# Optimization experiments

Measured on AMD Instinct MI355X. Metric: run time of the kernel, lower is better.

The kernel has to match this reference:

```python
import jax, jax.numpy as jnp
import numpy as np

N = 50000      # nodes
E = 800000     # edges
DIN = 128      # input feature dim
H = 4          # heads
D = 16         # per-head output dim
NEG_SLOPE = 0.2


def setup_inputs() -> dict:
    key = jax.random.key(0)
    k1, k2, k3, k4, k5, k6 = jax.random.split(key, 6)
    h = jax.random.normal(k1, (N, DIN), dtype=jnp.float32)
    W = jax.random.normal(k2, (DIN, H * D), dtype=jnp.float32) * 0.05
    attn_l = jax.random.normal(k3, (H, D), dtype=jnp.float32) * 0.1
    attn_r = jax.random.normal(k4, (H, D), dtype=jnp.float32) * 0.1
    src = jax.random.randint(k5, (E,), 0, N, dtype=jnp.int32)
    dst = jax.random.randint(k6, (E,), 0, N, dtype=jnp.int32)
    return {"h": h, "W": W, "attn_l": attn_l, "attn_r": attn_r, "src": src, "dst": dst}


def reference(h, W, attn_l, attn_r, src, dst):
    n = h.shape[0]
    # linear projection: [N, H, D]
    feat = (h @ W).reshape(n, H, D)
    # per-node attention halves: [N, H]
    el = jnp.einsum('nhd,hd->nh', feat, attn_l)
    er = jnp.einsum('nhd,hd->nh', feat, attn_r)
    # per-edge logits: [E, H]
    e = jax.nn.leaky_relu(el[src] + er[dst], negative_slope=NEG_SLOPE)
    # segment softmax grouped by destination node
    m = jax.ops.segment_max(e, dst, num_segments=n)          # [N, H]
    ex = jnp.exp(e - m[dst])                                  # [E, H]
    denom = jax.ops.segment_sum(ex, dst, num_segments=n)     # [N, H]
    a = ex / denom[dst]                                       # [E, H]
    # weighted aggregation of source features: [E, H, D] -> [N, H, D]
    msg = a[:, :, None] * feat[src]
    out = jax.ops.segment_sum(msg, dst, num_segments=n)
    # mean over heads (the wrapper's .mean(1)): [N, D]
    return out.mean(axis=1)
```

## Files before the change

### kernel.cpp

```cpp
#include <hip/hip_runtime.h>
#include <hip/hip_fp16.h>

#define NN   50000
#define EE   800000
#define KDIN 128
#define NH   4
#define ND   16
#define NEG_SLOPE 0.2f

#define NB        391
#define NBIN      128
#define CAP       2560
#define NNODE_PAD (NB * NBIN)
#define GSTRIDE   16
#define PB        196
#define PEB       4096
#define PROJ_ROWS 32
#define PROJ_LDP  130

__device__ __forceinline__ float lrelu(float x) {
    return x > 0.f ? x : NEG_SLOPE * x;
}
__device__ __forceinline__ float h2f(unsigned short u) {
    return __half2float(__ushort_as_half(u));
}

__global__ __launch_bounds__(256) void k_proj(
    const float* __restrict__ h, const float* __restrict__ W,
    const float* __restrict__ attn_l, const float* __restrict__ attn_r,
    unsigned short* __restrict__ feat_h, float* __restrict__ el, float* __restrict__ er,
    int* __restrict__ gcur)
{
    __shared__ float4 Wl[KDIN * 16];
    __shared__ float  hrow[PROJ_ROWS * PROJ_LDP];

    const int tid = threadIdx.x;
    if (blockIdx.x == 0) {
        for (int i = tid; i < NB * GSTRIDE; i += 256) gcur[i] = 0;
    }

    const float4* W4 = (const float4*)W;
    #pragma unroll
    for (int i = 0; i < 8; ++i) Wl[tid + 256 * i] = W4[tid + 256 * i];

    const int row_base = blockIdx.x * PROJ_ROWS;

    {
        const float4* h4 = (const float4*)h;
        #pragma unroll
        for (int i = 0; i < 4; ++i) {
            const int idx = tid + 256 * i;
            const int r   = idx >> 5;
            const int c   = idx & 31;
            int gr = row_base + r;
            if (gr >= NN) gr = NN - 1;
            float4 v = h4[(size_t)gr * 32 + c];
            *(float4*)&hrow[r * PROJ_LDP + c * 4] = v;
        }
    }
    __syncthreads();

    const int c4 = tid & 15;
    const int rg = tid >> 4;
    const float* row0 = &hrow[(rg * 2    ) * PROJ_LDP];
    const float* row1 = &hrow[(rg * 2 + 1) * PROJ_LDP];

    float4 a0 = make_float4(0.f, 0.f, 0.f, 0.f);
    float4 a1 = make_float4(0.f, 0.f, 0.f, 0.f);
    #pragma unroll 8
    for (int k = 0; k < KDIN; ++k) {
        const float4 w  = Wl[k * 16 + c4];
        const float  h0 = row0[k];
        const float  h1 = row1[k];
        a0.x = fmaf(h0, w.x, a0.x);
        a0.y = fmaf(h0, w.y, a0.y);
        a0.z = fmaf(h0, w.z, a0.z);
        a0.w = fmaf(h0, w.w, a0.w);
        a1.x = fmaf(h1, w.x, a1.x);
        a1.y = fmaf(h1, w.y, a1.y);
        a1.z = fmaf(h1, w.z, a1.z);
        a1.w = fmaf(h1, w.w, a1.w);
    }

    const int r0 = row_base + rg * 2;
    const int r1 = r0 + 1;

    ushort4 v0, v1;
    v0.x = __half_as_ushort(__float2half_rn(a0.x));
    v0.y = __half_as_ushort(__float2half_rn(a0.y));
    v0.z = __half_as_ushort(__float2half_rn(a0.z));
    v0.w = __half_as_ushort(__float2half_rn(a0.w));
    v1.x = __half_as_ushort(__float2half_rn(a1.x));
    v1.y = __half_as_ushort(__float2half_rn(a1.y));
    v1.z = __half_as_ushort(__float2half_rn(a1.z));
    v1.w = __half_as_ushort(__float2half_rn(a1.w));
    if (r0 < NN) ((ushort4*)feat_h)[(size_t)r0 * 16 + c4] = v0;
    if (r1 < NN) ((ushort4*)feat_h)[(size_t)r1 * 16 + c4] = v1;

    const float4 al = ((const float4*)attn_l)[c4];
    const float4 ar = ((const float4*)attn_r)[c4];
    float pl0 = a0.x*al.x + a0.y*al.y + a0.z*al.z + a0.w*al.w;
    float pr0 = a0.x*ar.x + a0.y*ar.y + a0.z*ar.z + a0.w*ar.w;
    float pl1 = a1.x*al.x + a1.y*al.y + a1.z*al.z + a1.w*al.w;
    float pr1 = a1.x*ar.x + a1.y*ar.y + a1.z*ar.z + a1.w*ar.w;
    pl0 += __shfl_xor(pl0, 1); pl0 += __shfl_xor(pl0, 2);
    pr0 += __shfl_xor(pr0, 1); pr0 += __shfl_xor(pr0, 2);
    pl1 += __shfl_xor(pl1, 1); pl1 += __shfl_xor(pl1, 2);
    pr1 += __shfl_xor(pr1, 1); pr1 += __shfl_xor(pr1, 2);
    if ((c4 & 3) == 0) {
        const int head = c4 >> 2;
        if (r0 < NN) { el[r0 * NH + head] = pl0; er[r0 * NH + head] = pr0; }
        if (r1 < NN) { el[r1 * NH + head] = pl1; er[r1 * NH + head] = pr1; }
    }
}

__global__ __launch_bounds__(512) void k_part(
    const int* __restrict__ src, const int* __restrict__ dst,
    int* __restrict__ gcur, unsigned int* __restrict__ pairs)
{
    __shared__ int lhist[NB];
    const int tid = threadIdx.x;
    const int eb  = blockIdx.x * PEB;

    unsigned int preg[8];
    int breg[8];
    for (int i = tid; i < NB; i += 512) lhist[i] = 0;
    __syncthreads();

    #pragma unroll
    for (int j = 0; j < 8; ++j) {
        const int e = eb + j * 512 + tid;
        if (e < EE) {
            const int d = dst[e];
            const int s = src[e];
            breg[j] = d >> 7;
            preg[j] = (unsigned int)s | ((unsigned int)(d & 127) << 16);
            atomicAdd(&lhist[breg[j]], 1);
        } else {
            breg[j] = -1;
        }
    }
    __syncthreads();

    for (int i = tid; i < NB; i += 512)
        lhist[i] = atomicAdd(&gcur[i * GSTRIDE], lhist[i]);
    __syncthreads();

    #pragma unroll
    for (int j = 0; j < 8; ++j) {
        if (breg[j] >= 0) {
            const int idx = atomicAdd(&lhist[breg[j]], 1);
            if (idx < CAP) pairs[breg[j] * CAP + idx] = preg[j];
        }
    }
}

__global__ __launch_bounds__(512) void k_lsort(
    const int* __restrict__ gcur, const unsigned int* __restrict__ pairs,
    unsigned short* __restrict__ sorted_src, unsigned int* __restrict__ rowinfo)
{
    __shared__ unsigned int buf[CAP];
    __shared__ int lhist[NBIN];
    __shared__ int lpre[NBIN];
    const int tid = threadIdx.x;
    const int b   = blockIdx.x;
    const int n   = min(gcur[b * GSTRIDE], CAP);

    if (tid < NBIN) lhist[tid] = 0;
    __syncthreads();

    for (int i = tid; i < n; i += 512) {
        const unsigned int p = pairs[b * CAP + i];
        buf[i] = p;
        atomicAdd(&lhist[(p >> 16) & 127], 1);
    }
    __syncthreads();

    if (tid < NBIN) lpre[tid] = lhist[tid];
    __syncthreads();
    #pragma unroll
    for (int off = 1; off < NBIN; off <<= 1) {
        int v = 0;
        if (tid < NBIN && tid >= off) v = lpre[tid - off];
        __syncthreads();
        if (tid < NBIN) lpre[tid] += v;
        __syncthreads();
    }

    if (tid < NBIN) {
        const int node = b * NBIN + tid;
        const int cnt  = lhist[tid];
        const int excl = lpre[tid] - cnt;
        rowinfo[node] = ((unsigned int)(b * CAP + excl) << 8) | (unsigned int)cnt;
        lhist[tid]    = excl;
    }
    __syncthreads();

    for (int i = tid; i < n; i += 512) {
        const unsigned int p = buf[i];
        const int r = atomicAdd(&lhist[(p >> 16) & 127], 1);
        sorted_src[b * CAP + r] = (unsigned short)(p & 0xFFFFu);
    }
}

__global__ __launch_bounds__(256) void k_gather(
    const float* __restrict__ el, const float* __restrict__ er,
    const unsigned short* __restrict__ feat_h,
    const unsigned short* __restrict__ sorted_src,
    const unsigned int* __restrict__ rowinfo,
    float* __restrict__ out)
{
    const int tid  = threadIdx.x;
    const int t    = blockIdx.x * 4 + (tid >> 6);
    const int lane = tid & 63;
    const int hd   = lane >> 4;

    const unsigned int info = rowinfo[t];
    const int base = (int)(info >> 8);
    const int n    = (int)(info & 255u);
    const float er_h = er[t * NH + hd];

    float acc = 0.f, dsum = 0.f;
    for (int j = 0; j < n; j += 8) {
        const int rem = n - j;
        int sq[8];
        #pragma unroll
        for (int q = 0; q < 8; ++q)
            sq[q] = (int)sorted_src[base + min(j + q, n - 1)];
        float xq[8], fq[8];
        #pragma unroll
        for (int q = 0; q < 8; ++q) xq[q] = el[sq[q] * NH + hd];
        #pragma unroll
        for (int q = 0; q < 8; ++q) fq[q] = h2f(feat_h[(size_t)sq[q] * 64 + lane]);
        #pragma unroll
        for (int q = 0; q < 8; ++q) {
            float e = __expf(lrelu(xq[q] + er_h));
            e = (q < rem) ? e : 0.f;
            dsum += e;
            acc = fmaf(e, fq[q], acc);
        }
    }

    float r = (n > 0) ? acc * __builtin_amdgcn_rcpf(dsum) : 0.f;
    r += __shfl_xor(r, 16);
    r += __shfl_xor(r, 32);
    if (lane < 16) out[t * ND + lane] = 0.25f * r;
}

extern "C" void kernel_launch(void* const* d_in, const int* in_sizes, int n_in,
                              void* d_out, int out_size, void* d_ws, size_t ws_size,
                              hipStream_t stream)
{
    const float* h  = (const float*)d_in[0];
    const float* W  = (const float*)d_in[1];
    const float* al = (const float*)d_in[2];
    const float* ar = (const float*)d_in[3];
    const int* src  = (const int*)d_in[4];
    const int* dst  = (const int*)d_in[5];
    float* out = (float*)d_out;

    unsigned short* feat_h = (unsigned short*)d_ws;
    float* el   = (float*)(feat_h + (size_t)NN * 64);
    float* er   = el + (size_t)NN * NH;
    int*   gcur = (int*)(er + (size_t)NN * NH);
    unsigned int* pairs = (unsigned int*)(gcur + NB * GSTRIDE);
    unsigned short* ssrc = (unsigned short*)(pairs + (size_t)NB * CAP);
    unsigned int* rowinfo = (unsigned int*)(ssrc + (size_t)NB * CAP);

    const int proj_blocks = (NN + PROJ_ROWS - 1) / PROJ_ROWS;
    k_proj  <<<proj_blocks, 256, 0, stream>>>(h, W, al, ar, feat_h, el, er, gcur);
    k_part  <<<PB,          512, 0, stream>>>(src, dst, gcur, pairs);
    k_lsort <<<NB,          512, 0, stream>>>(gcur, pairs, ssrc, rowinfo);
    k_gather<<<NN / 4,      256, 0, stream>>>(el, er, feat_h, ssrc, rowinfo, out);
}
```

Measured before the change: 144.9 us.

## Fuse local sort and gather into one kernel with LDS-resident sorted sources

Merges the per-bucket local sort and the per-node gather into a single kernel. The sorted source indices stay in shared memory, so the global sorted_src and rowinfo arrays and one launch go away. Buckets shrink to 64 nodes (782 blocks) so each block's sort fits in LDS and the prefix scan becomes one wavefront shuffle scan. The cost is fewer, larger gather blocks: 782 blocks of 4 waves, each wave looping over 16 nodes, where before there were 12500 blocks, which may lower latency hiding in the gather phase.

```diff
diff --git a/kernel.cpp b/kernel.cpp
--- a/kernel.cpp
+++ b/kernel.cpp
@@ -8,9 +8,9 @@
 #define ND   16
 #define NEG_SLOPE 0.2f
 
-#define NB        391
-#define NBIN      128
-#define CAP       2560
+#define NB        782
+#define NBIN      64
+#define CAP       1280
 #define NNODE_PAD (NB * NBIN)
 #define GSTRIDE   16
 #define PB        196
@@ -133,8 +133,8 @@
         if (e < EE) {
             const int d = dst[e];
             const int s = src[e];
-            breg[j] = d >> 7;
-            preg[j] = (unsigned int)s | ((unsigned int)(d & 127) << 16);
+            breg[j] = d >> 6;
+            preg[j] = (unsigned int)s | ((unsigned int)(d & 63) << 16);
             atomicAdd(&lhist[breg[j]], 1);
         } else {
             breg[j] = -1;
@@ -155,96 +155,88 @@
     }
 }
 
-__global__ __launch_bounds__(512) void k_lsort(
+__global__ __launch_bounds__(256) void k_lsg(
     const int* __restrict__ gcur, const unsigned int* __restrict__ pairs,
-    unsigned short* __restrict__ sorted_src, unsigned int* __restrict__ rowinfo)
-{
-    __shared__ unsigned int buf[CAP];
-    __shared__ int lhist[NBIN];
-    __shared__ int lpre[NBIN];
+    const float* __restrict__ el, const float* __restrict__ er,
+    const unsigned short* __restrict__ feat_h,
+    float* __restrict__ out)
+{
+    __shared__ unsigned int   buf[CAP];
+    __shared__ unsigned short ssrcL[CAP];
+    __shared__ int startL[NBIN], degL[NBIN], curL[NBIN];
+
     const int tid = threadIdx.x;
     const int b   = blockIdx.x;
     const int n   = min(gcur[b * GSTRIDE], CAP);
 
-    if (tid < NBIN) lhist[tid] = 0;
-    __syncthreads();
-
-    for (int i = tid; i < n; i += 512) {
+    if (tid < NBIN) curL[tid] = 0;
+    __syncthreads();
+
+    for (int i = tid; i < n; i += 256) {
         const unsigned int p = pairs[b * CAP + i];
         buf[i] = p;
-        atomicAdd(&lhist[(p >> 16) & 127], 1);
-    }
-    __syncthreads();
-
-    if (tid < NBIN) lpre[tid] = lhist[tid];
-    __syncthreads();
-    #pragma unroll
-    for (int off = 1; off < NBIN; off <<= 1) {
-        int v = 0;
-        if (tid < NBIN && tid >= off) v = lpre[tid - off];
-        __syncthreads();
-        if (tid < NBIN) lpre[tid] += v;
-        __syncthreads();
-    }
-
-    if (tid < NBIN) {
-        const int node = b * NBIN + tid;
-        const int cnt  = lhist[tid];
-        const int excl = lpre[tid] - cnt;
-        rowinfo[node] = ((unsigned int)(b * CAP + excl) << 8) | (unsigned int)cnt;
-        lhist[tid]    = excl;
-    }
-    __syncthreads();
-
-    for (int i = tid; i < n; i += 512) {
+        atomicAdd(&curL[(p >> 16) & 63], 1);
+    }
+    __syncthreads();
+
+    if (tid < 64) {
+        const int cnt = curL[tid];
+        int v = cnt;
+        #pragma unroll
+        for (int off = 1; off < 64; off <<= 1) {
+            const int u = __shfl_up(v, off);
+            if (tid >= off) v += u;
+        }
+        startL[tid] = v - cnt;
+        degL[tid]   = cnt;
+        curL[tid]   = v - cnt;
+    }
+    __syncthreads();
+
+    for (int i = tid; i < n; i += 256) {
         const unsigned int p = buf[i];
-        const int r = atomicAdd(&lhist[(p >> 16) & 127], 1);
-        sorted_src[b * CAP + r] = (unsigned short)(p & 0xFFFFu);
-    }
-}
-
-__global__ __launch_bounds__(256) void k_gather(
-    const float* __restrict__ el, const float* __restrict__ er,
-    const unsigned short* __restrict__ feat_h,
-    const unsigned short* __restrict__ sorted_src,
-    const unsigned int* __restrict__ rowinfo,
-    float* __restrict__ out)
-{
-    const int tid  = threadIdx.x;
-    const int t    = blockIdx.x * 4 + (tid >> 6);
+        const int r = atomicAdd(&curL[(p >> 16) & 63], 1);
+        ssrcL[r] = (unsigned short)(p & 0xFFFFu);
+    }
+    __syncthreads();
+
+    const int w    = tid >> 6;
     const int lane = tid & 63;
     const int hd   = lane >> 4;
 
-    const unsigned int info = rowinfo[t];
-    const int base = (int)(info >> 8);
-    const int n    = (int)(info & 255u);
-    const float er_h = er[t * NH + hd];
-
-    float acc = 0.f, dsum = 0.f;
-    for (int j = 0; j < n; j += 8) {
-        const int rem = n - j;
-        int sq[8];
-        #pragma unroll
-        for (int q = 0; q < 8; ++q)
-            sq[q] = (int)sorted_src[base + min(j + q, n - 1)];
-        float xq[8], fq[8];
-        #pragma unroll
-        for (int q = 0; q < 8; ++q) xq[q] = el[sq[q] * NH + hd];
-        #pragma unroll
-        for (int q = 0; q < 8; ++q) fq[q] = h2f(feat_h[(size_t)sq[q] * 64 + lane]);
-        #pragma unroll
-        for (int q = 0; q < 8; ++q) {
-            float e = __expf(lrelu(xq[q] + er_h));
-            e = (q < rem) ? e : 0.f;
-            dsum += e;
-            acc = fmaf(e, fq[q], acc);
-        }
-    }
-
-    float r = (n > 0) ? acc * __builtin_amdgcn_rcpf(dsum) : 0.f;
-    r += __shfl_xor(r, 16);
-    r += __shfl_xor(r, 32);
-    if (lane < 16) out[t * ND + lane] = 0.25f * r;
+    for (int ni = w; ni < NBIN; ni += 4) {
+        const int t = b * NBIN + ni;
+        if (t >= NN) continue;
+        const int base = startL[ni];
+        const int nd   = degL[ni];
+        const float er_h = er[t * NH + hd];
+
+        float acc = 0.f, dsum = 0.f;
+        for (int j = 0; j < nd; j += 8) {
+            const int rem = nd - j;
+            int sq[8];
+            #pragma unroll
+            for (int q = 0; q < 8; ++q)
+                sq[q] = (int)ssrcL[base + min(j + q, nd - 1)];
+            float xq[8], fq[8];
+            #pragma unroll
+            for (int q = 0; q < 8; ++q) xq[q] = el[sq[q] * NH + hd];
+            #pragma unroll
+            for (int q = 0; q < 8; ++q) fq[q] = h2f(feat_h[(size_t)sq[q] * 64 + lane]);
+            #pragma unroll
+            for (int q = 0; q < 8; ++q) {
+                float e = __expf(lrelu(xq[q] + er_h));
+                e = (q < rem) ? e : 0.f;
+                dsum += e;
+                acc = fmaf(e, fq[q], acc);
+            }
+        }
+
+        float r = (nd > 0) ? acc * __builtin_amdgcn_rcpf(dsum) : 0.f;
+        r += __shfl_xor(r, 16);
+        r += __shfl_xor(r, 32);
+        if (lane < 16) out[t * ND + lane] = 0.25f * r;
+    }
 }
 
 extern "C" void kernel_launch(void* const* d_in, const int* in_sizes, int n_in,
@@ -264,12 +256,9 @@
     float* er   = el + (size_t)NN * NH;
     int*   gcur = (int*)(er + (size_t)NN * NH);
     unsigned int* pairs = (unsigned int*)(gcur + NB * GSTRIDE);
-    unsigned short* ssrc = (unsigned short*)(pairs + (size_t)NB * CAP);
-    unsigned int* rowinfo = (unsigned int*)(ssrc + (size_t)NB * CAP);
 
     const int proj_blocks = (NN + PROJ_ROWS - 1) / PROJ_ROWS;
-    k_proj  <<<proj_blocks, 256, 0, stream>>>(h, W, al, ar, feat_h, el, er, gcur);
-    k_part  <<<PB,          512, 0, stream>>>(src, dst, gcur, pairs);
-    k_lsort <<<NB,          512, 0, stream>>>(gcur, pairs, ssrc, rowinfo);
-    k_gather<<<NN / 4,      256, 0, stream>>>(el, er, feat_h, ssrc, rowinfo, out);
-}
+    k_proj <<<proj_blocks, 256, 0, stream>>>(h, W, al, ar, feat_h, el, er, gcur);
+    k_part <<<PB,          512, 0, stream>>>(src, dst, gcur, pairs);
+    k_lsg  <<<NB,          256, 0, stream>>>(gcur, pairs, el, er, feat_h, out);
+}
```

New measurement: 155.6 us. 1.07x slower.
